# Kernel tuning notes

Measured on AMD Instinct MI355X. Metric: run time of the kernel, lower is better.

Reference implementation:

```python
import jax, jax.numpy as jnp
import numpy as np
from jax.scipy.special import erf

N = 4096        # n_points
M = 65536       # number of interaction events
T_MAX = 100.0   # observation window end
BETA0 = 1.0


def setup_inputs() -> dict:
    key = jax.random.key(0)
    k1, k2, k3, k4 = jax.random.split(key, 4)
    # data columns: [node_i, node_j, time] (indices stored as floats, as in the torch code)
    ij = jax.random.randint(k1, (M, 2), 0, N).astype(jnp.float32)
    times = jax.random.uniform(k2, (M,), minval=0.0, maxval=T_MAX)
    data = jnp.concatenate([ij, times[:, None]], axis=1)
    # learned parameters, initialized like the torch module
    z0 = jax.random.uniform(k3, (N, 2), dtype=jnp.float32) * 0.5
    v0 = jax.random.uniform(k4, (N, 2), dtype=jnp.float32) * 0.5
    beta = jnp.full((1, 1), BETA0, dtype=jnp.float32)
    t0 = jnp.float32(0.0)
    tn = jnp.float32(T_MAX)
    return {"data": data, "t0": t0, "tn": tn, "beta": beta, "z0": z0, "v0": v0}


def reference(data, t0, tn, beta, z0, v0):
    b = beta[0, 0]
    times = data[:, 2]                                   # (M,)
    i = jnp.floor(data[:, 0]).astype(jnp.int32)          # (M,)
    j = jnp.floor(data[:, 1]).astype(jnp.int32)          # (M,)

    # --- event term: log lambda_ij(t) = beta - ||z_i(t) - z_j(t)||^2, gathered per event.
    # (Identical to building the dense [N,N,M] tensor and fancy-indexing it.)
    zi = z0[i] + v0[i] * times[:, None]                  # (M,2)
    zj = z0[j] + v0[j] * times[:, None]                  # (M,2)
    d_event = jnp.sum((zi - zj) ** 2, axis=1)            # (M,)
    event_intensity = jnp.sum(b - d_event)

    # --- non-event term: closed-form integral of exp(beta - ||dz + dv*t||^2) over [t0, tn]
    # ||dz + dv t||^2 = a t^2 + bb t + c with a=|dv|^2, bb=2 dz.dv, c=|dz|^2
    dz = z0[:, None, :] - z0[None, :, :]                 # (N,N,2)
    dv = v0[:, None, :] - v0[None, :, :]                 # (N,N,2)
    a = jnp.sum(dv * dv, axis=-1)                        # (N,N)
    bb = 2.0 * jnp.sum(dz * dv, axis=-1)                 # (N,N)
    c = jnp.sum(dz * dz, axis=-1)                        # (N,N)
    a_safe = jnp.maximum(a, 1e-10)
    sqa = jnp.sqrt(a_safe)
    # exponent beta - (c - bb^2/(4a)) <= beta, numerically safe
    pref = (jnp.sqrt(jnp.pi) / (2.0 * sqa)) * jnp.exp(b + bb * bb / (4.0 * a_safe) - c)
    upper = erf(sqa * tn + bb / (2.0 * sqa))
    lower = erf(sqa * t0 + bb / (2.0 * sqa))
    integral = pref * (upper - lower)                    # (N,N)
    triu_mask = jnp.triu(jnp.ones((N, N), dtype=bool), k=1)
    non_event_intensity = jnp.sum(jnp.where(triu_mask, integral, 0.0))

    return event_intensity - non_event_intensity
```

## Files before the change

### kernel.cpp

```cpp
#include <hip/hip_runtime.h>


__device__ __forceinline__ float fast_erf_a(float x) {
    const float ax = __builtin_fabsf(x);
    const float t  = __builtin_amdgcn_rcpf(fmaf(0.3275911f, ax, 1.0f));
    float p = fmaf(t, 1.061405429f, -1.453152027f);
    p = fmaf(t, p, 1.421413741f);
    p = fmaf(t, p, -0.284496736f);
    p = fmaf(t, p, 0.254829592f);
    const float y = fmaf(-t * p, __expf(-ax * ax), 1.0f);
    return __builtin_copysignf(y, x);
}

__device__ __forceinline__ float fast_erf_b(float x) {
    const float ax = __builtin_fabsf(x);
    float p = fmaf(ax, 0.078108f, 0.000972f);
    p = fmaf(ax, p, 0.230389f);
    p = fmaf(ax, p, 0.278393f);
    p = fmaf(ax, p, 1.0f);
    const float w  = __builtin_amdgcn_rcpf(p);
    const float w2 = w * w;
    const float y  = fmaf(-w2, w2, 1.0f);
    return __builtin_copysignf(y, x);
}

__device__ __forceinline__ float erf_small(float x) {
    const float x2 = x * x;
    float p = fmaf(x2, 0.0052239776f, -0.0268661706f);
    p = fmaf(x2, p, 0.1128379167f);
    p = fmaf(x2, p, -0.3761263890f);
    p = fmaf(x2, p, 1.1283791671f);
    return x * p;
}

template<bool T0Z>
__device__ __forceinline__ float pair_rows(int r0, int r1, int N,
                                           const float2* __restrict__ z2,
                                           const float2* __restrict__ v2,
                                           float t0, float tn, float b) {
    const float SQRT_PI_OVER_2 = 0.88622692545275801f;
    float acc = 0.0f;
    #pragma unroll
    for (int r = 0; r < 2; ++r) {
        const int i = (r == 0) ? r0 : r1;
        if (r == 1 && r1 == r0) break;
        const float2 zi = z2[i];
        const float2 vi = v2[i];
        #pragma unroll 4
        for (int j = i + 1 + (int)threadIdx.x; j < N; j += 256) {
            const float2 zj = z2[j];
            const float2 vj = v2[j];
            const float dzx = zi.x - zj.x, dzy = zi.y - zj.y;
            const float dvx = vi.x - vj.x, dvy = vi.y - vj.y;

            const float a  = fmaf(dvx, dvx, dvy * dvy);
            const float du = fmaf(dzx, dvx, dzy * dvy);
            const float c  = fmaf(dzx, dzx, dzy * dzy);

            const float a_safe = fmaxf(a, 1e-10f);
            const float rsq = __builtin_amdgcn_rsqf(a_safe);
            const float sqa = a_safe * rsq;
            const float u   = du * rsq;

            const float pref  = SQRT_PI_OVER_2 * rsq * __expf(fmaf(u, u, b - c));
            const float upper = fast_erf_b(fmaf(sqa, tn, u));
            const float lower = T0Z ? erf_small(u)
                                    : fast_erf_a(fmaf(sqa, t0, u));
            acc += pref * (upper - lower);
        }
    }
    return acc;
}

__device__ __forceinline__ float block_reduce_add(float v) {
    __shared__ float smem[16];
    #pragma unroll
    for (int off = 32; off > 0; off >>= 1)
        v += __shfl_down(v, off, 64);
    const int lane = threadIdx.x & 63;
    const int wave = threadIdx.x >> 6;
    if (lane == 0) smem[wave] = v;
    __syncthreads();
    if (threadIdx.x == 0) {
        float s = smem[0];
        const int nw = (int)blockDim.x >> 6;
        for (int w = 1; w < nw; ++w) s += smem[w];
        return s;
    }
    return 0.0f;
}

__global__ void __launch_bounds__(256)
fused_kernel(const float* __restrict__ data,
             const float* __restrict__ t0p,
             const float* __restrict__ tnp,
             const float* __restrict__ beta,
             const float* __restrict__ z0,
             const float* __restrict__ v0,
             float* __restrict__ ws, int M, int N) {
    const float t0 = t0p[0];
    const float tn = tnp[0];
    const float b  = beta[0];
    const float2* __restrict__ z2 = (const float2*)z0;
    const float2* __restrict__ v2 = (const float2*)v0;

    float acc = 0.0f;

    const int chunk  = (M + (int)gridDim.x - 1) / (int)gridDim.x;
    const int mbeg   = (int)blockIdx.x * chunk;
    const int mend   = min(mbeg + chunk, M);
    for (int m = mbeg + (int)threadIdx.x; m < mend; m += 256) {
        const float fi = data[3 * m + 0];
        const float fj = data[3 * m + 1];
        const float t  = data[3 * m + 2];
        const int ii = (int)fi;
        const int jj = (int)fj;
        const float2 zi = z2[ii], zj = z2[jj];
        const float2 vi = v2[ii], vj = v2[jj];
        const float dx = (zi.x - zj.x) + (vi.x - vj.x) * t;
        const float dy = (zi.y - zj.y) + (vi.y - vj.y) * t;
        acc += b - (dx * dx + dy * dy);
    }

    const int r0 = (int)blockIdx.x;
    const int r1 = N - 1 - r0;

    float psum;
    if (t0 == 0.0f)
        psum = pair_rows<true >(r0, r1, N, z2, v2, t0, tn, b);
    else
        psum = pair_rows<false>(r0, r1, N, z2, v2, t0, tn, b);
    acc -= psum;

    const float s = block_reduce_add(acc);
    if (threadIdx.x == 0) ws[blockIdx.x] = s;
}

__global__ void __launch_bounds__(1024)
finalize_kernel(const float* __restrict__ ws, float* __restrict__ out,
                int nblocks) {
    const float4* __restrict__ ws4 = (const float4*)ws;
    const int n4 = nblocks >> 2;
    float v = 0.0f;
    for (int k = threadIdx.x; k < n4; k += 1024) {
        const float4 p = ws4[k];
        v += (p.x + p.y) + (p.z + p.w);
    }
    if (threadIdx.x == 0)
        for (int k = n4 << 2; k < nblocks; ++k) v += ws[k];
    const float s = block_reduce_add(v);
    if (threadIdx.x == 0) out[0] = s;
}

extern "C" void kernel_launch(void* const* d_in, const int* in_sizes, int n_in,
                              void* d_out, int out_size, void* d_ws, size_t ws_size,
                              hipStream_t stream) {
    const float* data = (const float*)d_in[0];
    const float* t0   = (const float*)d_in[1];
    const float* tn   = (const float*)d_in[2];
    const float* beta = (const float*)d_in[3];
    const float* z0   = (const float*)d_in[4];
    const float* v0   = (const float*)d_in[5];
    float* out = (float*)d_out;
    float* ws  = (float*)d_ws;

    const int M = in_sizes[0] / 3;
    const int N = in_sizes[4] / 2;

    const int blocks = (N + 1) / 2;
    fused_kernel<<<blocks, 256, 0, stream>>>(data, t0, tn, beta, z0, v0, ws, M, N);
    finalize_kernel<<<1, 1024, 0, stream>>>(ws, out, blocks);
}
```

Baseline: 77.96 us.

## Tile pair loop as 2 rows per j-load with split column halves

The pairwise loop now processes two adjacent rows (plus their mirrored pair) per loaded column element, so each z/v load of j is reused across two row evaluations. Each tile of four rows is split across two blocks by column parity, which keeps the block count the same while giving each thread more independent work. The event loop is moved after the pair work. This adds guard predicates and some wasted evaluations at the diagonal boundary in exchange for fewer global loads per pair and more ILP.

New measurement: 77.89 us. No clear change (-0.1%).

```diff
diff --git a/kernel.cpp b/kernel.cpp
--- a/kernel.cpp
+++ b/kernel.cpp
@@ -34,42 +34,27 @@
 }
 
 template<bool T0Z>
-__device__ __forceinline__ float pair_rows(int r0, int r1, int N,
-                                           const float2* __restrict__ z2,
-                                           const float2* __restrict__ v2,
+__device__ __forceinline__ float pair_eval(float2 zi, float2 vi,
+                                           float2 zj, float2 vj,
                                            float t0, float tn, float b) {
     const float SQRT_PI_OVER_2 = 0.88622692545275801f;
-    float acc = 0.0f;
-    #pragma unroll
-    for (int r = 0; r < 2; ++r) {
-        const int i = (r == 0) ? r0 : r1;
-        if (r == 1 && r1 == r0) break;
-        const float2 zi = z2[i];
-        const float2 vi = v2[i];
-        #pragma unroll 4
-        for (int j = i + 1 + (int)threadIdx.x; j < N; j += 256) {
-            const float2 zj = z2[j];
-            const float2 vj = v2[j];
-            const float dzx = zi.x - zj.x, dzy = zi.y - zj.y;
-            const float dvx = vi.x - vj.x, dvy = vi.y - vj.y;
+    const float dzx = zi.x - zj.x, dzy = zi.y - zj.y;
+    const float dvx = vi.x - vj.x, dvy = vi.y - vj.y;
 
-            const float a  = fmaf(dvx, dvx, dvy * dvy);
-            const float du = fmaf(dzx, dvx, dzy * dvy);
-            const float c  = fmaf(dzx, dzx, dzy * dzy);
+    const float a  = fmaf(dvx, dvx, dvy * dvy);
+    const float du = fmaf(dzx, dvx, dzy * dvy);
+    const float c  = fmaf(dzx, dzx, dzy * dzy);
 
-            const float a_safe = fmaxf(a, 1e-10f);
-            const float rsq = __builtin_amdgcn_rsqf(a_safe);
-            const float sqa = a_safe * rsq;
-            const float u   = du * rsq;
+    const float a_safe = fmaxf(a, 1e-10f);
+    const float rsq = __builtin_amdgcn_rsqf(a_safe);
+    const float sqa = a_safe * rsq;
+    const float u   = du * rsq;
 
-            const float pref  = SQRT_PI_OVER_2 * rsq * __expf(fmaf(u, u, b - c));
-            const float upper = fast_erf_b(fmaf(sqa, tn, u));
-            const float lower = T0Z ? erf_small(u)
-                                    : fast_erf_a(fmaf(sqa, t0, u));
-            acc += pref * (upper - lower);
-        }
-    }
-    return acc;
+    const float pref  = SQRT_PI_OVER_2 * rsq * __expf(fmaf(u, u, b - c));
+    const float upper = fast_erf_b(fmaf(sqa, tn, u));
+    const float lower = T0Z ? erf_small(u)
+                            : fast_erf_a(fmaf(sqa, t0, u));
+    return pref * (upper - lower);
 }
 
 __device__ __forceinline__ float block_reduce_add(float v) {
@@ -90,6 +75,43 @@
     return 0.0f;
 }
 
+template<bool T0Z>
+__device__ __forceinline__ float pair_tile(int q, int jofs, int N,
+                                           const float2* __restrict__ z2,
+                                           const float2* __restrict__ v2,
+                                           float t0, float tn, float b) {
+    const int i0 = 2 * q,      i1 = i0 + 1;
+    const int i2 = N - 2 - i0, i3 = i2 + 1;
+    const bool g1 = (i1 < N);
+    const bool g2 = (i2 > i1);
+    const bool g3 = (i3 > i1) && (i3 < N);
+
+    float a0 = 0.0f, a1 = 0.0f, a2 = 0.0f, a3 = 0.0f;
+
+    const float2 zi0 = z2[i0], vi0 = v2[i0];
+    const float2 zi1 = g1 ? z2[i1] : zi0, vi1 = g1 ? v2[i1] : vi0;
+    #pragma unroll 2
+    for (int j = i0 + 1 + jofs; j < N; j += 512) {
+        const float2 zj = z2[j], vj = v2[j];
+        a0 += pair_eval<T0Z>(zi0, vi0, zj, vj, t0, tn, b);
+        const float e1 = pair_eval<T0Z>(zi1, vi1, zj, vj, t0, tn, b);
+        a1 += (g1 && j > i1) ? e1 : 0.0f;
+    }
+
+    if (g2) {
+        const float2 zi2 = z2[i2], vi2 = v2[i2];
+        const float2 zi3 = g3 ? z2[i3] : zi2, vi3 = g3 ? v2[i3] : vi2;
+        #pragma unroll 2
+        for (int j = i2 + 1 + jofs; j < N; j += 512) {
+            const float2 zj = z2[j], vj = v2[j];
+            a2 += pair_eval<T0Z>(zi2, vi2, zj, vj, t0, tn, b);
+            const float e3 = pair_eval<T0Z>(zi3, vi3, zj, vj, t0, tn, b);
+            a3 += (g3 && j > i3) ? e3 : 0.0f;
+        }
+    }
+    return (a0 + a1) + (a2 + a3);
+}
+
 __global__ void __launch_bounds__(256)
 fused_kernel(const float* __restrict__ data,
              const float* __restrict__ t0p,
@@ -104,11 +126,18 @@
     const float2* __restrict__ z2 = (const float2*)z0;
     const float2* __restrict__ v2 = (const float2*)v0;
 
-    float acc = 0.0f;
+    const int q    = (int)blockIdx.x >> 1;
+    const int jofs = (((int)blockIdx.x & 1) << 8) + (int)threadIdx.x;
 
-    const int chunk  = (M + (int)gridDim.x - 1) / (int)gridDim.x;
-    const int mbeg   = (int)blockIdx.x * chunk;
-    const int mend   = min(mbeg + chunk, M);
+    float acc;
+    if (t0 == 0.0f)
+        acc = -pair_tile<true >(q, jofs, N, z2, v2, t0, tn, b);
+    else
+        acc = -pair_tile<false>(q, jofs, N, z2, v2, t0, tn, b);
+
+    const int chunk = (M + (int)gridDim.x - 1) / (int)gridDim.x;
+    const int mbeg  = (int)blockIdx.x * chunk;
+    const int mend  = min(mbeg + chunk, M);
     for (int m = mbeg + (int)threadIdx.x; m < mend; m += 256) {
         const float fi = data[3 * m + 0];
         const float fj = data[3 * m + 1];
@@ -121,16 +150,6 @@
         const float dy = (zi.y - zj.y) + (vi.y - vj.y) * t;
         acc += b - (dx * dx + dy * dy);
     }
-
-    const int r0 = (int)blockIdx.x;
-    const int r1 = N - 1 - r0;
-
-    float psum;
-    if (t0 == 0.0f)
-        psum = pair_rows<true >(r0, r1, N, z2, v2, t0, tn, b);
-    else
-        psum = pair_rows<false>(r0, r1, N, z2, v2, t0, tn, b);
-    acc -= psum;
 
     const float s = block_reduce_add(acc);
     if (threadIdx.x == 0) ws[blockIdx.x] = s;
@@ -167,7 +186,8 @@
     const int M = in_sizes[0] / 3;
     const int N = in_sizes[4] / 2;
 
-    const int blocks = (N + 1) / 2;
+    const int ntiles = (N + 3) / 4;
+    const int blocks = 2 * ntiles;
     fused_kernel<<<blocks, 256, 0, stream>>>(data, t0, tn, beta, z0, v0, ws, M, N);
     finalize_kernel<<<1, 1024, 0, stream>>>(ws, out, blocks);
 }
```
